# Optimization experiments

Measured on AMD Instinct MI355X. Metric: run time of the kernel, lower is better.

The kernel has to match this reference:

```python
import jax, jax.numpy as jnp
import numpy as np

B, C, D, H, W = 4, 128, 16, 16, 16
P = 64  # proj_dim (spatial branch is dead code in the original fusion; params omitted)


def setup_inputs() -> dict:
    key = jax.random.key(0)
    ks = jax.random.split(key, 10)
    lin = lambda k, o, i: 0.02 * jax.random.normal(k, (o, i), jnp.float32)
    return {
        "x": jax.random.normal(ks[0], (B, C, D, H, W), jnp.float32),
        "ln_g": jnp.ones((C,), jnp.float32),
        "ln_b": jnp.zeros((C,), jnp.float32),
        "Wq": lin(ks[1], C, C), "bq": jnp.zeros((C,), jnp.float32),
        "Wk": lin(ks[2], C, C), "bk": jnp.zeros((C,), jnp.float32),
        "Wvc": lin(ks[3], C, C), "bvc": jnp.zeros((C,), jnp.float32),
        "Wvch": lin(ks[4], C, C), "bvch": jnp.zeros((C,), jnp.float32),
        "Wconv": 0.02 * jax.random.normal(ks[5], (2, C, 3, 3, 3), jnp.float32),
        "bconv": jnp.zeros((2,), jnp.float32),
        "Wg": lin(ks[6], 3, C), "bg": jnp.zeros((3,), jnp.float32),
    }


def reference(x, ln_g, ln_b, Wq, bq, Wk, bk, Wvc, bvc, Wvch, bvch, Wconv, bconv, Wg, bg):
    b, c, d, h, w = x.shape
    n = d * h * w
    # LayerNorm over channels (permute to channels-last)
    xp = jnp.transpose(x, (0, 2, 3, 4, 1))                      # (B,D,H,W,C)
    mu = jnp.mean(xp, axis=-1, keepdims=True)
    var = jnp.mean((xp - mu) ** 2, axis=-1, keepdims=True)
    xn = (xp - mu) * jax.lax.rsqrt(var + 1e-5) * ln_g + ln_b     # (B,D,H,W,C)
    x_norm = jnp.transpose(xn, (0, 4, 1, 2, 3))                  # (B,C,D,H,W)
    # Causal Growth Field prediction: Conv3d C->2, k=3, SAME padding
    cgf = jax.lax.conv_general_dilated(
        x_norm, Wconv, (1, 1, 1), "SAME",
        dimension_numbers=("NCDHW", "OIDHW", "NCDHW")) + bconv[None, :, None, None, None]
    # Token sequence (B,N,C); same flattening order as x_norm.view(B,C,-1).transpose(1,2)
    xf = xn.reshape(b, n, c)
    q = jnp.einsum("bnc,oc->bno", xf, Wq) + bq
    k = jnp.einsum("bnc,oc->bno", xf, Wk) + bk
    # --- causal branch: full NxN attention ---
    vc = jnp.einsum("bnc,oc->bno", xf, Wvc) + bvc
    attn_causal = jax.nn.softmax(jnp.einsum("bnc,bmc->bnm", q, k) / (c ** 0.5), axis=-1)
    out_causal = jnp.einsum("bnm,bmc->bnc", attn_causal, vc)
    # --- channel branch: CxC attention ---
    vch = jnp.einsum("bnc,oc->bno", xf, Wvch) + bvch
    attn_channel = jax.nn.softmax(jnp.einsum("bnc,bnd->bcd", q, k) / (n ** 0.5), axis=-1)
    out_channel = jnp.einsum("bcd,bnd->bnc", attn_channel, vch)
    # --- gated fusion (original uses only weights 0 and 2; spatial branch is dead code) ---
    pooled = jnp.mean(x, axis=(2, 3, 4))                          # (B,C)
    weights = jax.nn.softmax(pooled @ Wg.T + bg, axis=-1)         # (B,3)
    fused = (weights[:, 0][:, None, None] * out_causal
             + weights[:, 2][:, None, None] * out_channel)        # (B,N,C)
    output = x + jnp.transpose(fused, (0, 2, 1)).reshape(b, c, d, h, w)
    return (output, cgf)
```

## Files before the change

kernel.cpp:

```cpp
#include <hip/hip_runtime.h>
#include <math.h>

#define CH   128
#define NSP  4096
#define BATCH 4
#define BIG  (BATCH*NSP*CH)
#define KCHUNKS 16
#define FKSPLIT 4
#define MB (1024*1024)

typedef short short8 __attribute__((ext_vector_type(8)));
typedef float floatx4 __attribute__((ext_vector_type(4)));

__device__ __forceinline__ unsigned short f2bu(float f) {
  union { float f; unsigned u; } v; v.f = f;
  unsigned r = v.u + 0x7fffu + ((v.u >> 16) & 1u);
  return (unsigned short)(r >> 16);
}
__device__ __forceinline__ float b2f(unsigned short h) {
  union { unsigned u; float f; } v; v.u = ((unsigned)h) << 16;
  return v.f;
}

__global__ __launch_bounds__(256) void ln_kernel(const float* __restrict__ x,
    const float* __restrict__ g, const float* __restrict__ bta,
    float* __restrict__ xf, unsigned short* __restrict__ xfb) {
  __shared__ float tile[128][65];
  __shared__ float pS[4][64];
  __shared__ float pQ[4][64];
  __shared__ float mu_s[64], rs_s[64];
  int t = threadIdx.x;
  int b  = blockIdx.x >> 6;
  int n0 = (blockIdx.x & 63) << 6;
  for (int i = t; i < 8192; i += 256) {
    int c = i >> 6, n = i & 63;
    tile[c][n] = x[(size_t)(b*CH + c)*NSP + n0 + n];
  }
  __syncthreads();
  {
    int n = t & 63, part = t >> 6;
    float s = 0.f, qq = 0.f;
    for (int c = part; c < 128; c += 4) { float v = tile[c][n]; s += v; qq += v*v; }
    pS[part][n] = s; pQ[part][n] = qq;
  }
  __syncthreads();
  if (t < 64) {
    float s = pS[0][t] + pS[1][t] + pS[2][t] + pS[3][t];
    float qq = pQ[0][t] + pQ[1][t] + pQ[2][t] + pQ[3][t];
    float mu = s * (1.f/128.f);
    float var = qq * (1.f/128.f) - mu*mu;
    mu_s[t] = mu;
    rs_s[t] = rsqrtf(var + 1e-5f);
  }
  __syncthreads();
  for (int i = t; i < 8192; i += 256) {
    int n = i >> 7, c = i & 127;
    float v = (tile[c][n] - mu_s[n]) * rs_s[n] * g[c] + bta[c];
    size_t idx = (size_t)(b*NSP + n0 + n)*CH + c;
    xf[idx] = v;
    xfb[idx] = f2bu(v);
  }
}

__global__ __launch_bounds__(256) void pooled_kernel(const float* __restrict__ x,
                                                     float* __restrict__ pooled) {
  int bc = blockIdx.x; int t = threadIdx.x;
  const float4* p = (const float4*)(x + (size_t)bc*NSP);
  float s = 0.f;
  for (int i = t; i < 1024; i += 256) { float4 v = p[i]; s += v.x+v.y+v.z+v.w; }
  for (int off = 32; off; off >>= 1) s += __shfl_xor(s, off, 64);
  __shared__ float red[4];
  if ((t & 63) == 0) red[t >> 6] = s;
  __syncthreads();
  if (t == 0) pooled[bc] = (red[0]+red[1]+red[2]+red[3]) * (1.f/4096.f);
}

__global__ void gate_kernel(const float* __restrict__ pooled, const float* __restrict__ Wg,
                            const float* __restrict__ bg, float* __restrict__ wgt) {
  __shared__ float lg[4][3];
  int t = threadIdx.x;
  if (t < 12) {
    int b = t / 3, j = t % 3;
    float s = bg[j];
    const float* pr = pooled + b*CH;
    const float* wr = Wg + j*CH;
    for (int c = 0; c < CH; ++c) s += pr[c]*wr[c];
    lg[b][j] = s;
  }
  __syncthreads();
  if (t < 4) {
    float a = lg[t][0], b2 = lg[t][1], c = lg[t][2];
    float m = fmaxf(a, fmaxf(b2, c));
    float e0 = __expf(a-m), e1 = __expf(b2-m), e2 = __expf(c-m);
    float inv = 1.f/(e0+e1+e2);
    wgt[t*3+0] = e0*inv; wgt[t*3+1] = e1*inv; wgt[t*3+2] = e2*inv;
  }
}

__global__ __launch_bounds__(256) void conv_kernel(const unsigned short* __restrict__ xfb,
    const float* __restrict__ Wc, const float* __restrict__ bc_, float* __restrict__ cgf) {
  __shared__ float Wl[27*256];
  int t = threadIdx.x;
  for (int i = t; i < 6912; i += 256) {
    int tap = i >> 8;
    int rem = i & 255;
    int o = rem >> 7, c = rem & 127;
    Wl[i] = Wc[o*3456 + c*27 + tap];
  }
  __syncthreads();
  int cg = t & 15, spl = t >> 4;
  int sp = blockIdx.x*16 + spl;
  int b = sp >> 12, n = sp & 4095;
  int z = n >> 8, y = (n >> 4) & 15, xw = n & 15;
  const unsigned short* xb = xfb + (size_t)b*NSP*CH + cg*8;
  float a0 = 0.f, a1 = 0.f;
  for (int kd = 0; kd < 3; ++kd) {
    int zz = z + kd - 1; if ((unsigned)zz >= 16u) continue;
    for (int kh = 0; kh < 3; ++kh) {
      int yy = y + kh - 1; if ((unsigned)yy >= 16u) continue;
      #pragma unroll
      for (int kw = 0; kw < 3; ++kw) {
        int xx = xw + kw - 1; if ((unsigned)xx >= 16u) continue;
        int nn = (zz << 8) + (yy << 4) + xx;
        short8 xv = *(const short8*)(xb + (size_t)nn*CH);
        int tap = (kd*3 + kh)*3 + kw;
        const float* wbase = &Wl[tap*256 + cg*8];
        float4 w00 = *(const float4*)(wbase);
        float4 w01 = *(const float4*)(wbase + 4);
        float4 w10 = *(const float4*)(wbase + 128);
        float4 w11 = *(const float4*)(wbase + 132);
        float x0 = b2f((unsigned short)xv[0]), x1 = b2f((unsigned short)xv[1]);
        float x2 = b2f((unsigned short)xv[2]), x3 = b2f((unsigned short)xv[3]);
        float x4 = b2f((unsigned short)xv[4]), x5 = b2f((unsigned short)xv[5]);
        float x6 = b2f((unsigned short)xv[6]), x7 = b2f((unsigned short)xv[7]);
        a0 += x0*w00.x + x1*w00.y + x2*w00.z + x3*w00.w
            + x4*w01.x + x5*w01.y + x6*w01.z + x7*w01.w;
        a1 += x0*w10.x + x1*w10.y + x2*w10.z + x3*w10.w
            + x4*w11.x + x5*w11.y + x6*w11.z + x7*w11.w;
      }
    }
  }
  #pragma unroll
  for (int off = 1; off <= 8; off <<= 1) {
    a0 += __shfl_xor(a0, off, 64);
    a1 += __shfl_xor(a1, off, 64);
  }
  if (cg == 0) {
    cgf[b*8192 + n]        = a0 + bc_[0];
    cgf[b*8192 + 4096 + n] = a1 + bc_[1];
  }
}

__global__ __launch_bounds__(256) void wcast_kernel(const float* __restrict__ Wq,
    const float* __restrict__ Wk, const float* __restrict__ Wvc,
    const float* __restrict__ Wvch, unsigned short* __restrict__ Wb) {
  int idx = blockIdx.x*256 + threadIdx.x;
  int pj = idx >> 14, wi = idx & 16383;
  const float* src = (pj == 0) ? Wq : (pj == 1) ? Wk : (pj == 2) ? Wvc : Wvch;
  Wb[idx] = f2bu(src[wi]);
}

__global__ __launch_bounds__(256) void proj_mfma_kernel(
    const unsigned short* __restrict__ xfb, const unsigned short* __restrict__ Wb,
    const float* __restrict__ bq, const float* __restrict__ bk,
    const float* __restrict__ bvc, const float* __restrict__ bvch,
    unsigned short* __restrict__ q, unsigned short* __restrict__ k,
    unsigned short* __restrict__ vc, unsigned short* __restrict__ vch) {
  __shared__ __align__(16) unsigned short Ws[128][136];
  int t = threadIdx.x;
  int lane = t & 63, w = t >> 6;
  int id = lane & 15, quad = lane >> 4;
  int pj = blockIdx.y;
  int r0 = blockIdx.x*128 + w*32;

  const unsigned short* Wp = Wb + ((size_t)pj << 14);
  for (int i = t; i < 2048; i += 256) {
    int rr = i >> 4, c8 = (i & 15) << 3;
    *(short8*)&Ws[rr][c8] = *(const short8*)(Wp + rr*CH + c8);
  }
  short8 af[2][4];
  #pragma unroll
  for (int m = 0; m < 2; ++m)
    #pragma unroll
    for (int kc = 0; kc < 4; ++kc)
      af[m][kc] = *(const short8*)(xfb + (size_t)(r0 + m*16 + id)*CH + kc*32 + quad*8);
  __syncthreads();

  floatx4 acc[2][8];
  #pragma unroll
  for (int m = 0; m < 2; ++m)
    #pragma unroll
    for (int nt = 0; nt < 8; ++nt) acc[m][nt] = (floatx4){0.f,0.f,0.f,0.f};
  #pragma unroll
  for (int nt = 0; nt < 8; ++nt)
    #pragma unroll
    for (int kc = 0; kc < 4; ++kc) {
      short8 bf = *(const short8*)&Ws[nt*16 + id][kc*32 + quad*8];
      acc[0][nt] = __builtin_amdgcn_mfma_f32_16x16x32_bf16(af[0][kc], bf, acc[0][nt], 0, 0, 0);
      acc[1][nt] = __builtin_amdgcn_mfma_f32_16x16x32_bf16(af[1][kc], bf, acc[1][nt], 0, 0, 0);
    }

  const float* bias = (pj == 0) ? bq : (pj == 1) ? bk : (pj == 2) ? bvc : bvch;
  unsigned short* Y = (pj == 0) ? q : (pj == 1) ? k : (pj == 2) ? vc : vch;
  #pragma unroll
  for (int nt = 0; nt < 8; ++nt) {
    float bsv = bias[nt*16 + id];
    #pragma unroll
    for (int m = 0; m < 2; ++m)
      #pragma unroll
      for (int r = 0; r < 4; ++r) {
        int row = r0 + m*16 + quad*4 + r;
        Y[(size_t)row*CH + nt*16 + id] = f2bu(acc[m][nt][r] + bsv);
      }
  }
}

__global__ __launch_bounds__(256) void vtrans_kernel(const unsigned short* __restrict__ vc,
                                                     unsigned short* __restrict__ vct) {
  __shared__ unsigned short T[128][72];
  int t = threadIdx.x;
  int b = blockIdx.x >> 6, n0 = (blockIdx.x & 63) << 6;
  for (int i = t; i < 1024; i += 256) {
    int n = i >> 4, c0 = (i & 15) << 3;
    short8 v = *(const short8*)&vc[(size_t)(b*NSP + n0 + n)*CH + c0];
    #pragma unroll
    for (int j = 0; j < 8; ++j) T[c0+j][n] = (unsigned short)v[j];
  }
  __syncthreads();
  for (int i = t; i < 1024; i += 256) {
    int c = i >> 3, k8 = (i & 7) << 3;
    *(short8*)&vct[((size_t)b*CH + c)*NSP + n0 + k8] = *(short8*)&T[c][k8];
  }
}

__global__ __launch_bounds__(256) void chscore_kernel(const unsigned short* __restrict__ q,
    const unsigned short* __restrict__ k, float* __restrict__ Sp) {
  __shared__ unsigned short Qt[128][72];
  __shared__ unsigned short Kt[128][72];
  int t = threadIdx.x;
  int lane = t & 63, w = t >> 6;
  int id = lane & 15, quad = lane >> 4;
  int p = blockIdx.x;
  int b = blockIdx.y;
  const unsigned short* qb = q + (size_t)b*NSP*CH;
  const unsigned short* kb = k + (size_t)b*NSP*CH;

  floatx4 acc[2][8];
  #pragma unroll
  for (int mt = 0; mt < 2; ++mt)
    #pragma unroll
    for (int nt = 0; nt < 8; ++nt) acc[mt][nt] = (floatx4){0.f,0.f,0.f,0.f};

  for (int s = 0; s < 4; ++s) {
    int nbase = p*256 + s*64;
    __syncthreads();
    #pragma unroll
    for (int it = 0; it < 4; ++it) {
      int task = t + it*256;
      int c = task & 127, r0 = (task >> 7) << 3;
      short8 vq, vk;
      #pragma unroll
      for (int j = 0; j < 8; ++j) {
        size_t off = (size_t)(nbase + r0 + j)*CH + c;
        vq[j] = (short)qb[off];
        vk[j] = (short)kb[off];
      }
      *(short8*)&Qt[c][r0] = vq;
      *(short8*)&Kt[c][r0] = vk;
    }
    __syncthreads();
    #pragma unroll
    for (int kc = 0; kc < 2; ++kc) {
      short8 af0 = *(const short8*)&Qt[w*32 + id     ][kc*32 + quad*8];
      short8 af1 = *(const short8*)&Qt[w*32 + 16 + id][kc*32 + quad*8];
      #pragma unroll
      for (int nt = 0; nt < 8; ++nt) {
        short8 bf = *(const short8*)&Kt[nt*16 + id][kc*32 + quad*8];
        acc[0][nt] = __builtin_amdgcn_mfma_f32_16x16x32_bf16(af0, bf, acc[0][nt], 0, 0, 0);
        acc[1][nt] = __builtin_amdgcn_mfma_f32_16x16x32_bf16(af1, bf, acc[1][nt], 0, 0, 0);
      }
    }
  }
  float* outp = Sp + ((size_t)(p*BATCH + b) << 14);
  #pragma unroll
  for (int mt = 0; mt < 2; ++mt)
    #pragma unroll
    for (int nt = 0; nt < 8; ++nt)
      #pragma unroll
      for (int r = 0; r < 4; ++r) {
        int c = w*32 + mt*16 + quad*4 + r;
        int d = nt*16 + id;
        outp[c*CH + d] = acc[mt][nt][r];
      }
}

__global__ __launch_bounds__(64) void chsoftmax_kernel(const float* __restrict__ Sp,
                                                       unsigned short* __restrict__ Sb) {
  int row = blockIdx.x;
  int b = row >> 7, c = row & 127;
  int t = threadIdx.x;
  float s0 = 0.f, s1 = 0.f;
  #pragma unroll 4
  for (int p = 0; p < KCHUNKS; ++p) {
    const float* r = Sp + (((size_t)(p*BATCH + b) << 7) + c)*CH;
    s0 += r[t]; s1 += r[t+64];
  }
  const float sc = 1.f/64.f;
  s0 *= sc; s1 *= sc;
  float m = fmaxf(s0, s1);
  for (int off = 32; off; off >>= 1) m = fmaxf(m, __shfl_xor(m, off, 64));
  float p0 = __expf(s0 - m), p1 = __expf(s1 - m);
  float s = p0 + p1;
  for (int off = 32; off; off >>= 1) s += __shfl_xor(s, off, 64);
  float inv = 1.f/s;
  unsigned short* r = Sb + (size_t)row*CH;
  r[t]    = f2bu(p0*inv);
  r[t+64] = f2bu(p1*inv);
}

__global__ __launch_bounds__(256) void chout_mfma_kernel(
    const unsigned short* __restrict__ vchb, const unsigned short* __restrict__ Sb,
    float* __restrict__ och) {
  __shared__ __align__(16) unsigned short As[128][136];
  int t = threadIdx.x;
  int lane = t & 63, w = t >> 6;
  int id = lane & 15, quad = lane >> 4;
  int b = blockIdx.x >> 5;
  int r0 = blockIdx.x*128 + w*32;

  const unsigned short* Sp = Sb + ((size_t)b << 14);
  for (int i = t; i < 2048; i += 256) {
    int rr = i >> 4, c8 = (i & 15) << 3;
    *(short8*)&As[rr][c8] = *(const short8*)(Sp + rr*CH + c8);
  }
  short8 af[2][4];
  #pragma unroll
  for (int m = 0; m < 2; ++m)
    #pragma unroll
    for (int kc = 0; kc < 4; ++kc)
      af[m][kc] = *(const short8*)(vchb + (size_t)(r0 + m*16 + id)*CH + kc*32 + quad*8);
  __syncthreads();

  floatx4 acc[2][8];
  #pragma unroll
  for (int m = 0; m < 2; ++m)
    #pragma unroll
    for (int nt = 0; nt < 8; ++nt) acc[m][nt] = (floatx4){0.f,0.f,0.f,0.f};
  #pragma unroll
  for (int nt = 0; nt < 8; ++nt)
    #pragma unroll
    for (int kc = 0; kc < 4; ++kc) {
      short8 bf = *(const short8*)&As[nt*16 + id][kc*32 + quad*8];
      acc[0][nt] = __builtin_amdgcn_mfma_f32_16x16x32_bf16(af[0][kc], bf, acc[0][nt], 0, 0, 0);
      acc[1][nt] = __builtin_amdgcn_mfma_f32_16x16x32_bf16(af[1][kc], bf, acc[1][nt], 0, 0, 0);
    }
  #pragma unroll
  for (int nt = 0; nt < 8; ++nt)
    #pragma unroll
    for (int m = 0; m < 2; ++m)
      #pragma unroll
      for (int r = 0; r < 4; ++r) {
        int row = r0 + m*16 + quad*4 + r;
        och[(size_t)row*CH + nt*16 + id] = acc[m][nt][r];
      }
}

__global__ __launch_bounds__(256) void flash_part_kernel(
    const unsigned short* __restrict__ Qg, const unsigned short* __restrict__ Kg,
    const unsigned short* __restrict__ Vtg,
    unsigned short* __restrict__ Opart, float* __restrict__ lpart) {
  __shared__ __align__(16) unsigned short Ks[64][136];
  __shared__ __align__(16) unsigned short Vt[128][72];
  __shared__ __align__(16) unsigned short Ps[4][32][68];
  int t = threadIdx.x;
  int lane = t & 63, w = t >> 6;
  int id = lane & 15, quad = lane >> 4;
  int blk = blockIdx.x;
  int x = blk & 7, y = blk >> 3;
  int tile = y & 31;
  int b = x >> 1;
  int ks = (x & 1) + ((y >> 5) << 1);
  int n0 = tile << 7;
  int r0 = n0 + w*32;

  const unsigned short* Qb = Qg  + (size_t)b*NSP*CH;
  const unsigned short* Kb = Kg  + (size_t)b*NSP*CH;
  const unsigned short* Vb = Vtg + (size_t)b*CH*NSP;

  short8 qf[2][4];
  #pragma unroll
  for (int m = 0; m < 2; ++m)
    #pragma unroll
    for (int kc = 0; kc < 4; ++kc)
      qf[m][kc] = *(const short8*)(Qb + (size_t)(r0 + m*16 + id)*CH + kc*32 + quad*8);

  floatx4 O[2][8];
  #pragma unroll
  for (int m = 0; m < 2; ++m)
    #pragma unroll
    for (int ct = 0; ct < 8; ++ct) O[m][ct] = (floatx4){0.f,0.f,0.f,0.f};
  float lrun[2][4];
  #pragma unroll
  for (int m = 0; m < 2; ++m)
    #pragma unroll
    for (int r = 0; r < 4; ++r) lrun[m][r] = 0.f;

  const float scale = 0.08838834764831845f;

  for (int kt = 0; kt < 16; ++kt) {
    int kbase = ks*1024 + kt*64;
    __syncthreads();
    #pragma unroll
    for (int it = 0; it < 4; ++it) {
      int task = t + it*256;
      int kr = task >> 4, kc8 = (task & 15) << 3;
      *(short8*)&Ks[kr][kc8] = *(const short8*)(Kb + (size_t)(kbase + kr)*CH + kc8);
      int vr = task >> 3, vn = (task & 7) << 3;
      *(short8*)&Vt[vr][vn] = *(const short8*)(Vb + (size_t)vr*NSP + kbase + vn);
    }
    __syncthreads();

    floatx4 S[2][4];
    #pragma unroll
    for (int nt = 0; nt < 4; ++nt) {
      floatx4 a0 = (floatx4){0.f,0.f,0.f,0.f};
      floatx4 a1 = (floatx4){0.f,0.f,0.f,0.f};
      #pragma unroll
      for (int kc = 0; kc < 4; ++kc) {
        short8 kf = *(const short8*)&Ks[nt*16 + id][kc*32 + quad*8];
        a0 = __builtin_amdgcn_mfma_f32_16x16x32_bf16(qf[0][kc], kf, a0, 0, 0, 0);
        a1 = __builtin_amdgcn_mfma_f32_16x16x32_bf16(qf[1][kc], kf, a1, 0, 0, 0);
      }
      S[0][nt] = a0; S[1][nt] = a1;
    }
    #pragma unroll
    for (int m = 0; m < 2; ++m) {
      float rs[4] = {0.f,0.f,0.f,0.f};
      #pragma unroll
      for (int nt = 0; nt < 4; ++nt)
        #pragma unroll
        for (int r = 0; r < 4; ++r) {
          float p = __expf(S[m][nt][r] * scale);
          rs[r] += p;
          Ps[w][m*16 + quad*4 + r][nt*16 + id] = f2bu(p);
        }
      #pragma unroll
      for (int off = 1; off <= 8; off <<= 1)
        #pragma unroll
        for (int r = 0; r < 4; ++r) rs[r] += __shfl_xor(rs[r], off, 64);
      #pragma unroll
      for (int r = 0; r < 4; ++r) lrun[m][r] += rs[r];
    }
    #pragma unroll
    for (int nc = 0; nc < 2; ++nc) {
      short8 pf0 = *(const short8*)&Ps[w][id     ][nc*32 + quad*8];
      short8 pf1 = *(const short8*)&Ps[w][16 + id][nc*32 + quad*8];
      #pragma unroll
      for (int ct = 0; ct < 8; ++ct) {
        short8 vf = *(const short8*)&Vt[ct*16 + id][nc*32 + quad*8];
        O[0][ct] = __builtin_amdgcn_mfma_f32_16x16x32_bf16(pf0, vf, O[0][ct], 0, 0, 0);
        O[1][ct] = __builtin_amdgcn_mfma_f32_16x16x32_bf16(pf1, vf, O[1][ct], 0, 0, 0);
      }
    }
  }

  unsigned short* Op = Opart + (size_t)ks*BIG + (size_t)b*NSP*CH;
  #pragma unroll
  for (int m = 0; m < 2; ++m)
    #pragma unroll
    for (int ct = 0; ct < 8; ++ct)
      #pragma unroll
      for (int r = 0; r < 4; ++r) {
        int row = r0 + m*16 + quad*4 + r;
        Op[(size_t)row*CH + ct*16 + id] = f2bu(O[m][ct][r]);
      }
  if (id == 0) {
    float* lp = lpart + (size_t)ks*BATCH*NSP + (size_t)b*NSP;
    #pragma unroll
    for (int m = 0; m < 2; ++m)
      #pragma unroll
      for (int r = 0; r < 4; ++r)
        lp[r0 + m*16 + quad*4 + r] = lrun[m][r];
  }
}

__global__ __launch_bounds__(256) void flash_combine_kernel(
    const unsigned short* __restrict__ Opart, const float* __restrict__ lpart,
    float* __restrict__ Oc) {
  size_t idx = (size_t)blockIdx.x*256 + threadIdx.x;
  size_t rowidx = idx >> 7;
  float o = 0.f, l = 0.f;
  #pragma unroll
  for (int p = 0; p < FKSPLIT; ++p) {
    o += b2f(Opart[(size_t)p*BIG + idx]);
    l += lpart[(size_t)p*BATCH*NSP + rowidx];
  }
  Oc[idx] = o / l;
}

__global__ __launch_bounds__(256) void fuse_kernel(const float* __restrict__ x,
    const float* __restrict__ oc, const float* __restrict__ och,
    const float* __restrict__ wgt, float* __restrict__ out) {
  __shared__ float T[128][65];
  int t = threadIdx.x;
  int b  = blockIdx.x >> 6;
  int n0 = (blockIdx.x & 63) << 6;
  float w0 = wgt[b*3 + 0], w2 = wgt[b*3 + 2];
  const float* ocb  = oc  + (size_t)(b*NSP + n0)*CH;
  const float* ochb = och + (size_t)(b*NSP + n0)*CH;
  for (int i = t; i < 8192; i += 256) {
    int n = i >> 7, c = i & 127;
    T[c][n] = w0*ocb[(size_t)n*CH + c] + w2*ochb[(size_t)n*CH + c];
  }
  __syncthreads();
  for (int i = t; i < 8192; i += 256) {
    int c = i >> 6, n = i & 63;
    size_t idx = (size_t)(b*CH + c)*NSP + n0 + n;
    out[idx] = x[idx] + T[c][n];
  }
}

extern "C" void kernel_launch(void* const* d_in, const int* in_sizes, int n_in,
                              void* d_out, int out_size, void* d_ws, size_t ws_size,
                              hipStream_t stream) {
  (void)in_sizes; (void)n_in; (void)out_size; (void)ws_size;
  const float* x     = (const float*)d_in[0];
  const float* ln_g  = (const float*)d_in[1];
  const float* ln_b  = (const float*)d_in[2];
  const float* Wq    = (const float*)d_in[3];
  const float* bq    = (const float*)d_in[4];
  const float* Wk    = (const float*)d_in[5];
  const float* bk    = (const float*)d_in[6];
  const float* Wvc   = (const float*)d_in[7];
  const float* bvc   = (const float*)d_in[8];
  const float* Wvch  = (const float*)d_in[9];
  const float* bvch  = (const float*)d_in[10];
  const float* Wconv = (const float*)d_in[11];
  const float* bconv = (const float*)d_in[12];
  const float* Wg    = (const float*)d_in[13];
  const float* bg    = (const float*)d_in[14];

  float* out = (float*)d_out;
  float* cgf = out + (size_t)BIG;

  char* base = (char*)d_ws;
  float* xf   = (float*)(base);
  float* och  = (float*)(base + 8*(size_t)MB);
  float* Sp             = (float*)(base + 16*(size_t)MB);
  unsigned short* vcb   = (unsigned short*)(base + 20*(size_t)MB);
  unsigned short* vchb  = (unsigned short*)(base + 28*(size_t)MB);
  unsigned short* Opart = (unsigned short*)(base + 16*(size_t)MB);
  float* lpart  = (float*)(base + 32*(size_t)MB);
  unsigned short* Schb = (unsigned short*)(base + 32*(size_t)MB + 256*1024);
  float* pooled = (float*)(base + 32*(size_t)MB + 512*1024);
  float* wgt    = pooled + BATCH*CH;
  unsigned short* qb  = (unsigned short*)(base + 33*(size_t)MB);
  unsigned short* kb  = (unsigned short*)(base + 37*(size_t)MB);
  unsigned short* vct = (unsigned short*)(base + 41*(size_t)MB);
  unsigned short* Wb  = (unsigned short*)(base + 45*(size_t)MB);
  unsigned short* xfb = (unsigned short*)(base + 46*(size_t)MB);

  ln_kernel     <<<256, 256, 0, stream>>>(x, ln_g, ln_b, xf, xfb);
  pooled_kernel <<<512, 256, 0, stream>>>(x, pooled);
  gate_kernel   <<<1,   64,  0, stream>>>(pooled, Wg, bg, wgt);
  wcast_kernel  <<<256, 256, 0, stream>>>(Wq, Wk, Wvc, Wvch, Wb);
  conv_kernel   <<<1024, 256, 0, stream>>>(xfb, Wconv, bconv, cgf);
  proj_mfma_kernel<<<dim3(128,4), 256, 0, stream>>>(xfb, Wb, bq, bk, bvc, bvch,
                                                    qb, kb, vcb, vchb);
  vtrans_kernel <<<256, 256, 0, stream>>>(vcb, vct);
  chscore_kernel<<<dim3(KCHUNKS, BATCH), 256, 0, stream>>>(qb, kb, Sp);
  chsoftmax_kernel<<<512, 64, 0, stream>>>(Sp, Schb);
  chout_mfma_kernel<<<128, 256, 0, stream>>>(vchb, Schb, och);
  flash_part_kernel<<<512, 256, 0, stream>>>(qb, kb, vct, Opart, lpart);
  flash_combine_kernel<<<BIG/256, 256, 0, stream>>>(Opart, lpart, xf );
  fuse_kernel   <<<256, 256, 0, stream>>>(x, xf, och, wgt, out);
}
```

Baseline: 247.3 us.

## Fuse flash combine into fuse kernel, rebalance flash split, widen channel-score grid

Removes the separate flash_combine kernel: fuse_kernel now sums the bf16 partial outputs and normalizers itself, so the fp32 causal output is no longer written to and read back from memory. The flash key dimension is split six ways (11/10 tiles each), giving 768 blocks instead of 512. chscore uses 64 chunks of 64 rows instead of 16 chunks of 256. LayerNorm stops writing the unused fp32 copy, and the workspace layout is reshuffled. In exchange there are more partial buffers to reduce, and more partial score matrices for chsoftmax to sum, whose hidden code must read KCHUNKS partials.

```diff
diff --git a/kernel.cpp b/kernel.cpp
--- a/kernel.cpp
+++ b/kernel.cpp
@@ -5,8 +5,8 @@
 #define NSP  4096
 #define BATCH 4
 #define BIG  (BATCH*NSP*CH)
-#define KCHUNKS 16
-#define FKSPLIT 4
+#define KCHUNKS 64
+#define FKSPLIT 6
 #define MB (1024*1024)
 
 typedef short short8 __attribute__((ext_vector_type(8)));
@@ -24,7 +24,7 @@
 
 __global__ __launch_bounds__(256) void ln_kernel(const float* __restrict__ x,
     const float* __restrict__ g, const float* __restrict__ bta,
-    float* __restrict__ xf, unsigned short* __restrict__ xfb) {
+    unsigned short* __restrict__ xfb) {
   __shared__ float tile[128][65];
   __shared__ float pS[4][64];
   __shared__ float pQ[4][64];
@@ -56,9 +56,7 @@
   for (int i = t; i < 8192; i += 256) {
     int n = i >> 7, c = i & 127;
     float v = (tile[c][n] - mu_s[n]) * rs_s[n] * g[c] + bta[c];
-    size_t idx = (size_t)(b*NSP + n0 + n)*CH + c;
-    xf[idx] = v;
-    xfb[idx] = f2bu(v);
+    xfb[(size_t)(b*NSP + n0 + n)*CH + c] = f2bu(v);
   }
 }
 
@@ -244,41 +242,38 @@
   int b = blockIdx.y;
   const unsigned short* qb = q + (size_t)b*NSP*CH;
   const unsigned short* kb = k + (size_t)b*NSP*CH;
+  int nbase = p*64;
+
+  #pragma unroll
+  for (int it = 0; it < 4; ++it) {
+    int task = t + it*256;
+    int c = task & 127, r0 = (task >> 7) << 3;
+    short8 vq, vk;
+    #pragma unroll
+    for (int j = 0; j < 8; ++j) {
+      size_t off = (size_t)(nbase + r0 + j)*CH + c;
+      vq[j] = (short)qb[off];
+      vk[j] = (short)kb[off];
+    }
+    *(short8*)&Qt[c][r0] = vq;
+    *(short8*)&Kt[c][r0] = vk;
+  }
+  __syncthreads();
 
   floatx4 acc[2][8];
   #pragma unroll
   for (int mt = 0; mt < 2; ++mt)
     #pragma unroll
     for (int nt = 0; nt < 8; ++nt) acc[mt][nt] = (floatx4){0.f,0.f,0.f,0.f};
-
-  for (int s = 0; s < 4; ++s) {
-    int nbase = p*256 + s*64;
-    __syncthreads();
-    #pragma unroll
-    for (int it = 0; it < 4; ++it) {
-      int task = t + it*256;
-      int c = task & 127, r0 = (task >> 7) << 3;
-      short8 vq, vk;
-      #pragma unroll
-      for (int j = 0; j < 8; ++j) {
-        size_t off = (size_t)(nbase + r0 + j)*CH + c;
-        vq[j] = (short)qb[off];
-        vk[j] = (short)kb[off];
-      }
-      *(short8*)&Qt[c][r0] = vq;
-      *(short8*)&Kt[c][r0] = vk;
-    }
-    __syncthreads();
-    #pragma unroll
-    for (int kc = 0; kc < 2; ++kc) {
-      short8 af0 = *(const short8*)&Qt[w*32 + id     ][kc*32 + quad*8];
-      short8 af1 = *(const short8*)&Qt[w*32 + 16 + id][kc*32 + quad*8];
-      #pragma unroll
-      for (int nt = 0; nt < 8; ++nt) {
-        short8 bf = *(const short8*)&Kt[nt*16 + id][kc*32 + quad*8];
-        acc[0][nt] = __builtin_amdgcn_mfma_f32_16x16x32_bf16(af0, bf, acc[0][nt], 0, 0, 0);
-        acc[1][nt] = __builtin_amdgcn_mfma_f32_16x16x32_bf16(af1, bf, acc[1][nt], 0, 0, 0);
-      }
+  #pragma unroll
+  for (int kc = 0; kc < 2; ++kc) {
+    short8 af0 = *(const short8*)&Qt[w*32 + id     ][kc*32 + quad*8];
+    short8 af1 = *(const short8*)&Qt[w*32 + 16 + id][kc*32 + quad*8];
+    #pragma unroll
+    for (int nt = 0; nt < 8; ++nt) {
+      short8 bf = *(const short8*)&Kt[nt*16 + id][kc*32 + quad*8];
+      acc[0][nt] = __builtin_amdgcn_mfma_f32_16x16x32_bf16(af0, bf, acc[0][nt], 0, 0, 0);
+      acc[1][nt] = __builtin_amdgcn_mfma_f32_16x16x32_bf16(af1, bf, acc[1][nt], 0, 0, 0);
     }
   }
   float* outp = Sp + ((size_t)(p*BATCH + b) << 14);
@@ -376,10 +371,12 @@
   int lane = t & 63, w = t >> 6;
   int id = lane & 15, quad = lane >> 4;
   int blk = blockIdx.x;
-  int x = blk & 7, y = blk >> 3;
-  int tile = y & 31;
-  int b = x >> 1;
-  int ks = (x & 1) + ((y >> 5) << 1);
+  int tile = blk & 31;
+  int g = blk >> 5;
+  int b = g & 3;
+  int ks = g >> 2;
+  int ksoff = (ks < 4) ? ks*11 : 44 + (ks - 4)*10;
+  int kcnt  = (ks < 4) ? 11 : 10;
   int n0 = tile << 7;
   int r0 = n0 + w*32;
 
@@ -407,8 +404,8 @@
 
   const float scale = 0.08838834764831845f;
 
-  for (int kt = 0; kt < 16; ++kt) {
-    int kbase = ks*1024 + kt*64;
+  for (int kt = 0; kt < kcnt; ++kt) {
+    int kbase = (ksoff + kt)*64;
     __syncthreads();
     #pragma unroll
     for (int it = 0; it < 4; ++it) {
@@ -484,33 +481,32 @@
   }
 }
 
-__global__ __launch_bounds__(256) void flash_combine_kernel(
+__global__ __launch_bounds__(256) void fuse_kernel(const float* __restrict__ x,
     const unsigned short* __restrict__ Opart, const float* __restrict__ lpart,
-    float* __restrict__ Oc) {
-  size_t idx = (size_t)blockIdx.x*256 + threadIdx.x;
-  size_t rowidx = idx >> 7;
-  float o = 0.f, l = 0.f;
-  #pragma unroll
-  for (int p = 0; p < FKSPLIT; ++p) {
-    o += b2f(Opart[(size_t)p*BIG + idx]);
-    l += lpart[(size_t)p*BATCH*NSP + rowidx];
-  }
-  Oc[idx] = o / l;
-}
-
-__global__ __launch_bounds__(256) void fuse_kernel(const float* __restrict__ x,
-    const float* __restrict__ oc, const float* __restrict__ och,
-    const float* __restrict__ wgt, float* __restrict__ out) {
+    const float* __restrict__ och, const float* __restrict__ wgt,
+    float* __restrict__ out) {
   __shared__ float T[128][65];
+  __shared__ float linv[64];
   int t = threadIdx.x;
   int b  = blockIdx.x >> 6;
   int n0 = (blockIdx.x & 63) << 6;
   float w0 = wgt[b*3 + 0], w2 = wgt[b*3 + 2];
-  const float* ocb  = oc  + (size_t)(b*NSP + n0)*CH;
+  if (t < 64) {
+    float l = 0.f;
+    #pragma unroll
+    for (int p = 0; p < FKSPLIT; ++p)
+      l += lpart[(size_t)p*BATCH*NSP + b*NSP + n0 + t];
+    linv[t] = 1.f / l;
+  }
+  __syncthreads();
   const float* ochb = och + (size_t)(b*NSP + n0)*CH;
   for (int i = t; i < 8192; i += 256) {
     int n = i >> 7, c = i & 127;
-    T[c][n] = w0*ocb[(size_t)n*CH + c] + w2*ochb[(size_t)n*CH + c];
+    size_t oidx = (size_t)(b*NSP + n0 + n)*CH + c;
+    float o = 0.f;
+    #pragma unroll
+    for (int p = 0; p < FKSPLIT; ++p) o += b2f(Opart[(size_t)p*BIG + oidx]);
+    T[c][n] = w0*o*linv[n] + w2*ochb[(size_t)n*CH + c];
   }
   __syncthreads();
   for (int i = t; i < 8192; i += 256) {
@@ -544,23 +540,22 @@
   float* cgf = out + (size_t)BIG;
 
   char* base = (char*)d_ws;
-  float* xf   = (float*)(base);
-  float* och  = (float*)(base + 8*(size_t)MB);
-  float* Sp             = (float*)(base + 16*(size_t)MB);
-  unsigned short* vcb   = (unsigned short*)(base + 20*(size_t)MB);
-  unsigned short* vchb  = (unsigned short*)(base + 28*(size_t)MB);
-  unsigned short* Opart = (unsigned short*)(base + 16*(size_t)MB);
+  float* och  = (float*)(base);
+  unsigned short* Opart = (unsigned short*)(base + 8*(size_t)MB);
+  float* Sp             = (float*)(base + 8*(size_t)MB);
+  unsigned short* vcb   = (unsigned short*)(base + 24*(size_t)MB);
   float* lpart  = (float*)(base + 32*(size_t)MB);
-  unsigned short* Schb = (unsigned short*)(base + 32*(size_t)MB + 256*1024);
-  float* pooled = (float*)(base + 32*(size_t)MB + 512*1024);
+  unsigned short* Schb = (unsigned short*)(base + 32*(size_t)MB + 512*1024);
+  float* pooled = (float*)(base + 32*(size_t)MB + 768*1024);
   float* wgt    = pooled + BATCH*CH;
-  unsigned short* qb  = (unsigned short*)(base + 33*(size_t)MB);
-  unsigned short* kb  = (unsigned short*)(base + 37*(size_t)MB);
-  unsigned short* vct = (unsigned short*)(base + 41*(size_t)MB);
-  unsigned short* Wb  = (unsigned short*)(base + 45*(size_t)MB);
-  unsigned short* xfb = (unsigned short*)(base + 46*(size_t)MB);
-
-  ln_kernel     <<<256, 256, 0, stream>>>(x, ln_g, ln_b, xf, xfb);
+  unsigned short* qb   = (unsigned short*)(base + 33*(size_t)MB);
+  unsigned short* kb   = (unsigned short*)(base + 37*(size_t)MB);
+  unsigned short* vct  = (unsigned short*)(base + 41*(size_t)MB);
+  unsigned short* vchb = (unsigned short*)(base + 45*(size_t)MB);
+  unsigned short* Wb   = (unsigned short*)(base + 49*(size_t)MB);
+  unsigned short* xfb  = (unsigned short*)(base + 49*(size_t)MB + 256*1024);
+
+  ln_kernel     <<<256, 256, 0, stream>>>(x, ln_g, ln_b, xfb);
   pooled_kernel <<<512, 256, 0, stream>>>(x, pooled);
   gate_kernel   <<<1,   64,  0, stream>>>(pooled, Wg, bg, wgt);
   wcast_kernel  <<<256, 256, 0, stream>>>(Wq, Wk, Wvc, Wvch, Wb);
@@ -571,7 +566,6 @@
   chscore_kernel<<<dim3(KCHUNKS, BATCH), 256, 0, stream>>>(qb, kb, Sp);
   chsoftmax_kernel<<<512, 64, 0, stream>>>(Sp, Schb);
   chout_mfma_kernel<<<128, 256, 0, stream>>>(vchb, Schb, och);
-  flash_part_kernel<<<512, 256, 0, stream>>>(qb, kb, vct, Opart, lpart);
-  flash_combine_kernel<<<BIG/256, 256, 0, stream>>>(Opart, lpart, xf );
-  fuse_kernel   <<<256, 256, 0, stream>>>(x, xf, och, wgt, out);
-}
+  flash_part_kernel<<<768, 256, 0, stream>>>(qb, kb, vct, Opart, lpart);
+  fuse_kernel   <<<256, 256, 0, stream>>>(x, Opart, lpart, och, wgt, out);
+}
```

Measured after the change: 266.0 us. 1.08x slower.
